# Performance work log

Hardware: AMD Instinct MI355X
Metric: run time of the kernel (lower is better)

Reference implementation:

```python
import jax, jax.numpy as jnp
import numpy as np

IN, H, OUT = 8, 256, 24  # input_size, hidden_size, output_size
B, T = 2048, 256


def _gate_step(hx, x, Wx, Wh, b):
    # Fused version of the 8 per-gate Linears: one [.,IN]@[IN,4H] + one [.,H]@[H,4H]
    gates = x @ Wx + hx @ Wh + b            # [B, 4H]
    i, f, o, g = jnp.split(gates, 4, axis=-1)
    i, f, o = jax.nn.sigmoid(i), jax.nn.sigmoid(f), jax.nn.sigmoid(o)
    g = jnp.tanh(g)
    # NOTE: in the original code cx is never reassigned, so it stays zeros and
    # cy = cx*f + i*g == i*g on every step. We replicate that exactly.
    cy = i * g
    return o * jnp.tanh(cy)


def setup_inputs() -> dict:
    key = jax.random.key(0)
    ks = jax.random.split(key, 9)
    s = 0.05
    return {
        "inputs0": jax.random.normal(ks[0], (B, T, IN), jnp.float32),
        "inputs1": jax.random.normal(ks[1], (B, OUT - 1), jnp.float32),
        # concatenated gate weights, order [i | f | o | c]
        "Wx": jax.random.normal(ks[2], (IN, 4 * H), jnp.float32) * s,
        "Wh": jax.random.normal(ks[3], (H, 4 * H), jnp.float32) * s,
        "b": jax.random.normal(ks[4], (4 * H,), jnp.float32) * s,  # bx + bh folded
        "Wy": jax.random.normal(ks[5], (H, 1), jnp.float32) * s,
        "by": jax.random.normal(ks[6], (1,), jnp.float32) * s,
        # fresh random Linear(1, IN) per decoder step in the original -> per-step params
        "dec_w": jax.random.normal(ks[7], (OUT - 1, IN), jnp.float32) * s,
        "dec_b": jax.random.normal(ks[8], (OUT - 1, IN), jnp.float32) * s,
    }


def reference(inputs0, inputs1, Wx, Wh, b, Wy, by, dec_w, dec_b):
    bsz = inputs0.shape[0]
    h0 = jnp.zeros((bsz, H), inputs0.dtype)

    # ---- encoder: scan over time (strict recurrence) ----
    x_seq = jnp.transpose(inputs0, (1, 0, 2))  # [T, B, IN]

    def enc_step(h, x):
        return _gate_step(h, x, Wx, Wh, b), None

    h, _ = jax.lax.scan(enc_step, h0, x_seq)
    hy0 = h @ Wy + by                           # [B, 1]

    # ---- decoder: OUT-1 steps, each with its own fresh 1->IN linear ----
    x1_seq = jnp.transpose(inputs1, (1, 0))[: OUT - 1]  # [OUT-1, B]

    def dec_step(h, inp):
        x1, w, bb = inp
        x = x1[:, None] * w[None, :] + bb[None, :]      # [B, IN]
        h = _gate_step(h, x, Wx, Wh, b)
        return h, h @ Wy + by                            # y: [B, 1]

    _, ys = jax.lax.scan(dec_step, h, (x1_seq, dec_w, dec_b))  # ys: [OUT-1, B, 1]

    hy = jnp.concatenate([hy0, jnp.transpose(ys[..., 0], (1, 0))], axis=1)  # [B, OUT]
    return hy
```

## Files before the change

### kernel.cpp

```cpp
#include <hip/hip_runtime.h>


typedef short bf16x8 __attribute__((ext_vector_type(8)));
typedef float f32x4 __attribute__((ext_vector_type(4)));

#define T_ENC 256
#define N_DEC 23
#define NSTEP 279
#define HSTR 296
#define PV_T 28
#define PA_T 8
#define LDS_T 18

__device__ __forceinline__ short f2bf(float f) {
  unsigned u = __float_as_uint(f);
  u = (u + 0x7fffu + ((u >> 16) & 1u)) >> 16;
  return (short)u;
}
__device__ __forceinline__ float bf2f(short s) {
  return __uint_as_float(((unsigned)(unsigned short)s) << 16);
}

#if __has_builtin(__builtin_amdgcn_rcpf)
#define RCPF(x) __builtin_amdgcn_rcpf(x)
#else
#define RCPF(x) (1.0f / (x))
#endif

__device__ __forceinline__ float sigm(float x) { return RCPF(1.0f + __expf(-x)); }
__device__ __forceinline__ float tanhf_fast(float x) {
  return 1.0f - 2.0f * RCPF(__expf(2.0f * x) + 1.0f);
}

__global__ void pack_kernel(const float* __restrict__ Wx, const float* __restrict__ Wh,
                            const float* __restrict__ b, short* __restrict__ Wpack) {
  int tau = blockIdx.x;
  int l = threadIdx.x;
  int n_tile = tau / 9, kt = tau % 9;
  int w = n_tile / 6, t = n_tile % 6;
  int gate = t >> 1, loc = t & 1;
  int base = (gate == 0) ? 0 : (gate == 1 ? 512 : 768);
  int c = l & 15, q = l >> 4;
  int oc = base + w * 32 + loc * 16 + c;
  bf16x8 v;
#pragma unroll
  for (int e = 0; e < 8; ++e) {
    int k = kt * 32 + q * 8 + e;
    float f;
    if (k < 256)       f = Wh[k * 1024 + oc];
    else if (k < 264)  f = Wx[(k - 256) * 1024 + oc];
    else if (k == 264) f = b[oc];
    else               f = 0.0f;
    v[e] = f2bf(f);
  }
  ((bf16x8*)Wpack)[tau * 64 + l] = v;
}

__global__ __launch_bounds__(512, 2) void lstm_kernel(
    const float* __restrict__ inputs0, const float* __restrict__ inputs1,
    const float* __restrict__ Wy, const float* __restrict__ by,
    const float* __restrict__ dec_w, const float* __restrict__ dec_b,
    const short* __restrict__ Wpack, float* __restrict__ out) {
  __shared__ __align__(16) short B_lds[8 * LDS_T * 512];
  __shared__ __align__(16) short hbuf[2][8 * HSTR];
  __shared__ float Wy_lds[256];
  __shared__ float ypart[128];

  const int tid = threadIdx.x;
  const int wg = blockIdx.x;
  const int lane = tid & 63;
  const int w = tid >> 6;
  const int q = lane >> 4;
  const int c = lane & 15;

  const bf16x8* wp = (const bf16x8*)Wpack;

  bf16x8 Bv[PV_T];
#pragma unroll
  for (int r = 0; r < PV_T; ++r) {
    bf16x8 t0 = wp[(w * 54 + r) * 64 + lane];
    asm("" : "=v"(Bv[r]) : "0"(t0));
  }
  bf16x8 Ba[PA_T];
#pragma unroll
  for (int r = 0; r < PA_T; ++r) {
    bf16x8 t0 = wp[(w * 54 + PV_T + r) * 64 + lane];
    asm("" : "=a"(Ba[r]) : "0"(t0));
  }
#pragma unroll
  for (int j = 0; j < LDS_T; ++j) {
    bf16x8 v = wp[(w * 54 + PV_T + PA_T + j) * 64 + lane];
    *(bf16x8*)(B_lds + (w * LDS_T + j) * 512 + lane * 8) = v;
  }

  for (int i = tid; i < 2 * 8 * HSTR; i += 512) hbuf[0][i] = 0;
  if (tid < 256) Wy_lds[tid] = Wy[tid];
  __syncthreads();

  if (tid < 64) {
    int m = tid >> 3, kk = tid & 7;
    hbuf[0][m * HSTR + 256 + kk] = f2bf(inputs0[((wg * 8 + m) * 256 + 0) * 8 + kk]);
  }
  if (tid < 16)
    hbuf[tid >> 3][(tid & 7) * HSTR + 264] = (short)0x3F80;
  const float byv = by[0];
  __syncthreads();

#define LDSB(j) (*(const bf16x8*)(B_lds + (w * LDS_T + (j)) * 512 + lane * 8))

  const int qh = q >> 1;
  const int row0 = (q & 1) * 4;
  const int colw = w * 32 + qh * 16 + c;

  for (int s = 0; s < NSTEP; ++s) {
    const short* hc = &hbuf[s & 1][0];
    short* hn = &hbuf[(s + 1) & 1][0];

    float xv = 0.0f;
    const bool do_x = (tid < 64) && (s + 1 < NSTEP);
    const int xm = tid >> 3, xk = tid & 7;
    if (do_x) {
      int sn = s + 1;
      if (sn < T_ENC) {
        xv = inputs0[((wg * 8 + xm) * 256 + sn) * 8 + xk];
      } else {
        int d = sn - T_ENC;
        xv = inputs1[(wg * 8 + xm) * N_DEC + d] * dec_w[d * 8 + xk] + dec_b[d * 8 + xk];
      }
    }

    bf16x8 A[9];
#pragma unroll
    for (int kt = 0; kt < 9; ++kt)
      A[kt] = *(const bf16x8*)(hc + (c & 7) * HSTR + kt * 32 + q * 8);

    f32x4 a0, a1;
    a0[0]=0.f;a0[1]=0.f;a0[2]=0.f;a0[3]=0.f; a1=a0;
#pragma unroll
    for (int kt = 0; kt < 9; ++kt) {
      a0 = __builtin_amdgcn_mfma_f32_16x16x32_bf16(A[kt], Bv[kt], a0, 0, 0, 0);
      a1 = __builtin_amdgcn_mfma_f32_16x16x32_bf16(A[kt], Bv[9 + kt], a1, 0, 0, 0);
    }
    float ii[4];
    {
      const f32x4 vi = qh ? a1 : a0;
#pragma unroll
      for (int j = 0; j < 4; ++j) ii[j] = sigm(vi[j]);
    }

    a0[0]=0.f;a0[1]=0.f;a0[2]=0.f;a0[3]=0.f; a1=a0;
#pragma unroll
    for (int kt = 0; kt < 9; ++kt) {
      a0 = __builtin_amdgcn_mfma_f32_16x16x32_bf16(A[kt], Bv[18 + kt], a0, 0, 0, 0);
      if (kt == 0)
        a1 = __builtin_amdgcn_mfma_f32_16x16x32_bf16(A[kt], Bv[27], a1, 0, 0, 0);
      else
        a1 = __builtin_amdgcn_mfma_f32_16x16x32_bf16(A[kt], Ba[kt - 1], a1, 0, 0, 0);
    }
    float oo[4];
    {
      const f32x4 vo = qh ? a1 : a0;
#pragma unroll
      for (int j = 0; j < 4; ++j) oo[j] = sigm(vo[j]);
    }

    a0[0]=0.f;a0[1]=0.f;a0[2]=0.f;a0[3]=0.f; a1=a0;
#pragma unroll
    for (int kt = 0; kt < 9; ++kt) {
      a0 = __builtin_amdgcn_mfma_f32_16x16x32_bf16(A[kt], LDSB(kt), a0, 0, 0, 0);
      a1 = __builtin_amdgcn_mfma_f32_16x16x32_bf16(A[kt], LDSB(9 + kt), a1, 0, 0, 0);
    }
    float hh[4];
    {
      const f32x4 vg = qh ? a1 : a0;
#pragma unroll
      for (int j = 0; j < 4; ++j) {
        float gg = tanhf_fast(vg[j]);
        hh[j] = oo[j] * tanhf_fast(ii[j] * gg);
      }
    }
    {
      unsigned pk01, pk23;
      asm("v_cvt_pk_bf16_f32 %0, %1, %2" : "=v"(pk01) : "v"(hh[0]), "v"(hh[1]));
      asm("v_cvt_pk_bf16_f32 %0, %1, %2" : "=v"(pk23) : "v"(hh[2]), "v"(hh[3]));
      hn[(row0 + 0) * HSTR + colw] = (short)(pk01 & 0xffffu);
      hn[(row0 + 1) * HSTR + colw] = (short)(pk01 >> 16);
      hn[(row0 + 2) * HSTR + colw] = (short)(pk23 & 0xffffu);
      hn[(row0 + 3) * HSTR + colw] = (short)(pk23 >> 16);
    }
    if (do_x) hn[xm * HSTR + 256 + xk] = f2bf(xv);
    __syncthreads();

    if (s >= T_ENC - 1) {
      if (tid < 128) {
        int m = tid & 7, kq = tid >> 3;
        const short* hp = hn + m * HSTR + kq * 16;
        bf16x8 h0 = *(const bf16x8*)(hp);
        bf16x8 h1 = *(const bf16x8*)(hp + 8);
        float part = 0.0f;
#pragma unroll
        for (int j = 0; j < 8; ++j) {
          part += bf2f(h0[j]) * Wy_lds[kq * 16 + j];
          part += bf2f(h1[j]) * Wy_lds[kq * 16 + 8 + j];
        }
        ypart[tid] = part;
      }
      __syncthreads();
      if (tid < 8) {
        float y = byv;
#pragma unroll
        for (int kq = 0; kq < 16; ++kq) y += ypart[kq * 8 + tid];
        out[(wg * 8 + tid) * 24 + (s - (T_ENC - 1))] = y;
      }
      __syncthreads();
    }
  }
}

extern "C" void kernel_launch(void* const* d_in, const int* in_sizes, int n_in,
                              void* d_out, int out_size, void* d_ws, size_t ws_size,
                              hipStream_t stream) {
  const float* inputs0 = (const float*)d_in[0];
  const float* inputs1 = (const float*)d_in[1];
  const float* Wx      = (const float*)d_in[2];
  const float* Wh      = (const float*)d_in[3];
  const float* b       = (const float*)d_in[4];
  const float* Wy      = (const float*)d_in[5];
  const float* by      = (const float*)d_in[6];
  const float* dec_w   = (const float*)d_in[7];
  const float* dec_b   = (const float*)d_in[8];

  short* Wpack = (short*)d_ws;

  pack_kernel<<<dim3(432), dim3(64), 0, stream>>>(Wx, Wh, b, Wpack);
  lstm_kernel<<<dim3(256), dim3(512), 0, stream>>>(
      inputs0, inputs1, Wy, by, dec_w, dec_b, Wpack, (float*)d_out);
}
```

Measured before the change: 432.6 us.

## Store hidden state in MFMA-fragment LDS layout and fold exp scaling into weights

Replaces the row-major padded hidden-state buffer with a layout that matches the MFMA A-fragment order, so each lane reads its operand as one contiguous 16-byte LDS load per k-tile, aiming to cut bank conflicts on the per-step recurrence. The log2(e) factors for sigmoid and tanh are pre-multiplied into the packed weights, which lets the kernel call exp2 directly and drop a multiply per activation. It also seeds the first MFMA of each chain from a shared zero accumulator and raises wave priority around the MFMA blocks. Scaling before bf16 rounding changes numerics slightly, and the Wy readout indexing had to be remapped to the new layout.

```diff
diff --git a/kernel.cpp b/kernel.cpp
--- a/kernel.cpp
+++ b/kernel.cpp
@@ -7,10 +7,10 @@
 #define T_ENC 256
 #define N_DEC 23
 #define NSTEP 279
-#define HSTR 296
 #define PV_T 28
 #define PA_T 8
 #define LDS_T 18
+#define AFRAG 2304
 
 __device__ __forceinline__ short f2bf(float f) {
   unsigned u = __float_as_uint(f);
@@ -26,11 +26,11 @@
 #else
 #define RCPF(x) (1.0f / (x))
 #endif
-
-__device__ __forceinline__ float sigm(float x) { return RCPF(1.0f + __expf(-x)); }
-__device__ __forceinline__ float tanhf_fast(float x) {
-  return 1.0f - 2.0f * RCPF(__expf(2.0f * x) + 1.0f);
-}
+#if __has_builtin(__builtin_amdgcn_exp2f)
+#define EXP2(x) __builtin_amdgcn_exp2f(x)
+#else
+#define EXP2(x) __exp2f(x)
+#endif
 
 __global__ void pack_kernel(const float* __restrict__ Wx, const float* __restrict__ Wh,
                             const float* __restrict__ b, short* __restrict__ Wpack) {
@@ -40,6 +40,7 @@
   int w = n_tile / 6, t = n_tile % 6;
   int gate = t >> 1, loc = t & 1;
   int base = (gate == 0) ? 0 : (gate == 1 ? 512 : 768);
+  float scale = (gate == 2) ? 2.885390082f : 1.442695041f;
   int c = l & 15, q = l >> 4;
   int oc = base + w * 32 + loc * 16 + c;
   bf16x8 v;
@@ -51,7 +52,7 @@
     else if (k < 264)  f = Wx[(k - 256) * 1024 + oc];
     else if (k == 264) f = b[oc];
     else               f = 0.0f;
-    v[e] = f2bf(f);
+    v[e] = f2bf(f * scale);
   }
   ((bf16x8*)Wpack)[tau * 64 + l] = v;
 }
@@ -62,7 +63,7 @@
     const float* __restrict__ dec_w, const float* __restrict__ dec_b,
     const short* __restrict__ Wpack, float* __restrict__ out) {
   __shared__ __align__(16) short B_lds[8 * LDS_T * 512];
-  __shared__ __align__(16) short hbuf[2][8 * HSTR];
+  __shared__ __align__(16) short A_lds[2][AFRAG];
   __shared__ float Wy_lds[256];
   __shared__ float ypart[128];
 
@@ -93,16 +94,14 @@
     *(bf16x8*)(B_lds + (w * LDS_T + j) * 512 + lane * 8) = v;
   }
 
-  for (int i = tid; i < 2 * 8 * HSTR; i += 512) hbuf[0][i] = 0;
+  for (int i = tid; i < 2 * AFRAG; i += 512) A_lds[0][i] = 0;
   if (tid < 256) Wy_lds[tid] = Wy[tid];
   __syncthreads();
 
-  if (tid < 64) {
-    int m = tid >> 3, kk = tid & 7;
-    hbuf[0][m * HSTR + 256 + kk] = f2bf(inputs0[((wg * 8 + m) * 256 + 0) * 8 + kk]);
-  }
+  if (tid < 64)
+    A_lds[0][2048 + tid] = f2bf(inputs0[((wg * 8 + (tid >> 3)) * 256 + 0) * 8 + (tid & 7)]);
   if (tid < 16)
-    hbuf[tid >> 3][(tid & 7) * HSTR + 264] = (short)0x3F80;
+    A_lds[tid >> 3][2112 + (tid & 7) * 8] = (short)0x3F80;
   const float byv = by[0];
   __syncthreads();
 
@@ -110,17 +109,21 @@
 
   const int qh = q >> 1;
   const int row0 = (q & 1) * 4;
-  const int colw = w * 32 + qh * 16 + c;
+  const int woff = w * 256 + (qh * 2 + (c >> 3)) * 64 + row0 * 8 + (c & 7);
+  const int abase = q * 64 + (c & 7) * 8;
+
+  f32x4 z4;
+  z4[0] = 0.f; z4[1] = 0.f; z4[2] = 0.f; z4[3] = 0.f;
+  asm("" : "+v"(z4));
 
   for (int s = 0; s < NSTEP; ++s) {
-    const short* hc = &hbuf[s & 1][0];
-    short* hn = &hbuf[(s + 1) & 1][0];
+    const short* Ab = &A_lds[s & 1][0];
+    short* An = &A_lds[(s + 1) & 1][0];
 
     float xv = 0.0f;
     const bool do_x = (tid < 64) && (s + 1 < NSTEP);
-    const int xm = tid >> 3, xk = tid & 7;
     if (do_x) {
-      int sn = s + 1;
+      int sn = s + 1, xm = tid >> 3, xk = tid & 7;
       if (sn < T_ENC) {
         xv = inputs0[((wg * 8 + xm) * 256 + sn) * 8 + xk];
       } else {
@@ -132,71 +135,76 @@
     bf16x8 A[9];
 #pragma unroll
     for (int kt = 0; kt < 9; ++kt)
-      A[kt] = *(const bf16x8*)(hc + (c & 7) * HSTR + kt * 32 + q * 8);
-
-    f32x4 a0, a1;
-    a0[0]=0.f;a0[1]=0.f;a0[2]=0.f;a0[3]=0.f; a1=a0;
-#pragma unroll
-    for (int kt = 0; kt < 9; ++kt) {
+      A[kt] = *(const bf16x8*)(Ab + kt * 256 + abase);
+
+    __builtin_amdgcn_s_setprio(1);
+    f32x4 a0 = __builtin_amdgcn_mfma_f32_16x16x32_bf16(A[0], Bv[0], z4, 0, 0, 0);
+    f32x4 a1 = __builtin_amdgcn_mfma_f32_16x16x32_bf16(A[0], Bv[9], z4, 0, 0, 0);
+#pragma unroll
+    for (int kt = 1; kt < 9; ++kt) {
       a0 = __builtin_amdgcn_mfma_f32_16x16x32_bf16(A[kt], Bv[kt], a0, 0, 0, 0);
       a1 = __builtin_amdgcn_mfma_f32_16x16x32_bf16(A[kt], Bv[9 + kt], a1, 0, 0, 0);
     }
+    __builtin_amdgcn_s_setprio(0);
     float ii[4];
     {
       const f32x4 vi = qh ? a1 : a0;
 #pragma unroll
-      for (int j = 0; j < 4; ++j) ii[j] = sigm(vi[j]);
-    }
-
-    a0[0]=0.f;a0[1]=0.f;a0[2]=0.f;a0[3]=0.f; a1=a0;
-#pragma unroll
-    for (int kt = 0; kt < 9; ++kt) {
+      for (int j = 0; j < 4; ++j) ii[j] = RCPF(1.0f + EXP2(-vi[j]));
+    }
+
+    __builtin_amdgcn_s_setprio(1);
+    a0 = __builtin_amdgcn_mfma_f32_16x16x32_bf16(A[0], Bv[18], z4, 0, 0, 0);
+    a1 = __builtin_amdgcn_mfma_f32_16x16x32_bf16(A[0], Bv[27], z4, 0, 0, 0);
+#pragma unroll
+    for (int kt = 1; kt < 9; ++kt) {
       a0 = __builtin_amdgcn_mfma_f32_16x16x32_bf16(A[kt], Bv[18 + kt], a0, 0, 0, 0);
-      if (kt == 0)
-        a1 = __builtin_amdgcn_mfma_f32_16x16x32_bf16(A[kt], Bv[27], a1, 0, 0, 0);
-      else
-        a1 = __builtin_amdgcn_mfma_f32_16x16x32_bf16(A[kt], Ba[kt - 1], a1, 0, 0, 0);
-    }
+      a1 = __builtin_amdgcn_mfma_f32_16x16x32_bf16(A[kt], Ba[kt - 1], a1, 0, 0, 0);
+    }
+    __builtin_amdgcn_s_setprio(0);
     float oo[4];
     {
       const f32x4 vo = qh ? a1 : a0;
 #pragma unroll
-      for (int j = 0; j < 4; ++j) oo[j] = sigm(vo[j]);
-    }
-
-    a0[0]=0.f;a0[1]=0.f;a0[2]=0.f;a0[3]=0.f; a1=a0;
-#pragma unroll
-    for (int kt = 0; kt < 9; ++kt) {
+      for (int j = 0; j < 4; ++j) oo[j] = RCPF(1.0f + EXP2(-vo[j]));
+    }
+
+    __builtin_amdgcn_s_setprio(1);
+    a0 = __builtin_amdgcn_mfma_f32_16x16x32_bf16(A[0], LDSB(0), z4, 0, 0, 0);
+    a1 = __builtin_amdgcn_mfma_f32_16x16x32_bf16(A[0], LDSB(9), z4, 0, 0, 0);
+#pragma unroll
+    for (int kt = 1; kt < 9; ++kt) {
       a0 = __builtin_amdgcn_mfma_f32_16x16x32_bf16(A[kt], LDSB(kt), a0, 0, 0, 0);
       a1 = __builtin_amdgcn_mfma_f32_16x16x32_bf16(A[kt], LDSB(9 + kt), a1, 0, 0, 0);
     }
-    float hh[4];
+    __builtin_amdgcn_s_setprio(0);
     {
       const f32x4 vg = qh ? a1 : a0;
+      unsigned pk01, pk23;
+      float hh[4];
 #pragma unroll
       for (int j = 0; j < 4; ++j) {
-        float gg = tanhf_fast(vg[j]);
-        hh[j] = oo[j] * tanhf_fast(ii[j] * gg);
-      }
-    }
-    {
-      unsigned pk01, pk23;
+        float gg = 1.0f - 2.0f * RCPF(EXP2(vg[j]) + 1.0f);
+        float cy = ii[j] * gg;
+        float t2 = 1.0f - 2.0f * RCPF(EXP2(cy * 2.885390082f) + 1.0f);
+        hh[j] = oo[j] * t2;
+      }
       asm("v_cvt_pk_bf16_f32 %0, %1, %2" : "=v"(pk01) : "v"(hh[0]), "v"(hh[1]));
       asm("v_cvt_pk_bf16_f32 %0, %1, %2" : "=v"(pk23) : "v"(hh[2]), "v"(hh[3]));
-      hn[(row0 + 0) * HSTR + colw] = (short)(pk01 & 0xffffu);
-      hn[(row0 + 1) * HSTR + colw] = (short)(pk01 >> 16);
-      hn[(row0 + 2) * HSTR + colw] = (short)(pk23 & 0xffffu);
-      hn[(row0 + 3) * HSTR + colw] = (short)(pk23 >> 16);
-    }
-    if (do_x) hn[xm * HSTR + 256 + xk] = f2bf(xv);
+      An[woff + 0 * 8] = (short)(pk01 & 0xffffu);
+      An[woff + 1 * 8] = (short)(pk01 >> 16);
+      An[woff + 2 * 8] = (short)(pk23 & 0xffffu);
+      An[woff + 3 * 8] = (short)(pk23 >> 16);
+    }
+    if (do_x) An[2048 + tid] = f2bf(xv);
     __syncthreads();
 
     if (s >= T_ENC - 1) {
       if (tid < 128) {
         int m = tid & 7, kq = tid >> 3;
-        const short* hp = hn + m * HSTR + kq * 16;
+        const short* hp = An + (kq >> 1) * 256 + (kq & 1) * 128 + m * 8;
         bf16x8 h0 = *(const bf16x8*)(hp);
-        bf16x8 h1 = *(const bf16x8*)(hp + 8);
+        bf16x8 h1 = *(const bf16x8*)(hp + 64);
         float part = 0.0f;
 #pragma unroll
         for (int j = 0; j < 8; ++j) {
```

Result: no change. 424.4 us (-1.9%).
